# Kernel tuning notes

Hardware: AMD Instinct MI355X
Metric: run time of the kernel (lower is better)

## Reference

```python
import jax, jax.numpy as jnp
import numpy as np

N, E, B, F, H = 50000, 600000, 256, 128, 128
RATIO = 0.8
BN_EPS = 1e-5


def _topk_keep(score, batch, mask):
    # Per-graph top-ceil(RATIO*live) selection, expressed as a fixed-size keep mask.
    s = jnp.where(mask, score, -jnp.inf)
    order = jnp.lexsort((-s, batch))  # primary: batch id, secondary: score desc
    rank = jnp.zeros(N, dtype=jnp.int32).at[order].set(jnp.arange(N, dtype=jnp.int32))
    total = jax.ops.segment_sum(jnp.ones(N, dtype=jnp.int32), batch, B)
    starts = jnp.cumsum(total) - total
    r_in_g = (rank - starts[batch]).astype(jnp.float32)  # rank within own graph
    live = jax.ops.segment_sum(mask.astype(jnp.float32), batch, B)
    k = jnp.ceil(RATIO * live)
    return (r_in_g < k[batch]) & mask


def _forward(x, edge_index, batch, W1s, b1s, W2s, b2s, gammas, betas, pool_ws):
    src, dst = edge_index[0], edge_index[1]
    mask = jnp.ones(N, dtype=bool)      # live-node mask (TopK pooling shrinks graphs)
    e_mask = jnp.ones(E, dtype=bool)    # live-edge mask
    out = jnp.zeros((B, 2 * H), dtype=x.dtype)
    for i in range(4):
        # GINConv (eps=0): MLP(x + sum_{j->i} x_j)
        msg = jnp.where(e_mask[:, None], x[src], 0.0)
        agg = jax.ops.segment_sum(msg, dst, num_segments=N)
        h = x + agg
        h = jax.nn.relu(h @ W1s[i] + b1s[i]) @ W2s[i] + b2s[i]
        # BatchNorm (training mode) over live nodes only
        m = mask[:, None].astype(h.dtype)
        n = jnp.maximum(jnp.sum(m), 1.0)
        mean = jnp.sum(h * m, axis=0) / n
        var = jnp.sum(((h - mean) ** 2) * m, axis=0) / n
        h = (h - mean) * jax.lax.rsqrt(var + BN_EPS) * gammas[i] + betas[i]
        h = jax.nn.relu(h) * m
        # TopKPooling(ratio=0.8): score = x@w/||w||, keep top-k per graph, scale by tanh
        w = pool_ws[i]
        score = (h @ w) / jnp.linalg.norm(w)
        keep = _topk_keep(score, batch, mask)
        x = jnp.where(keep[:, None], h * jnp.tanh(score)[:, None], 0.0)
        mask = keep
        e_mask = e_mask & keep[src] & keep[dst]
        # global max pool + global mean pool over live nodes
        mx = jax.ops.segment_max(jnp.where(mask[:, None], x, -jnp.inf), batch, num_segments=B)
        mx = jnp.where(jnp.isfinite(mx), mx, 0.0)
        cnt = jax.ops.segment_sum(mask.astype(x.dtype), batch, num_segments=B)
        mn = jax.ops.segment_sum(x, batch, num_segments=B) / jnp.maximum(cnt, 1.0)[:, None]
        out = out + jnp.concatenate([mx, mn], axis=1)  # x1 + x2 + x3 + x4
    return out


def setup_inputs() -> dict:
    key = jax.random.key(0)
    k = jax.random.split(key, 8)
    s = 1.0 / np.sqrt(H)
    return {
        "x": jax.random.normal(k[0], (N, F), jnp.float32),
        "edge_index": jax.random.randint(k[1], (2, E), 0, N),
        "batch": jnp.sort(jax.random.randint(k[2], (N,), 0, B)),
        "W1s": jax.random.normal(k[3], (4, F, H), jnp.float32) * s,
        "b1s": jax.random.normal(k[4], (4, H), jnp.float32) * s,
        "W2s": jax.random.normal(k[5], (4, H, H), jnp.float32) * s,
        "b2s": jax.random.normal(k[6], (4, H), jnp.float32) * s,
        "gammas": jnp.ones((4, H), jnp.float32),
        "betas": jnp.zeros((4, H), jnp.float32),
        "pool_ws": jax.random.normal(k[7], (4, H), jnp.float32) * s,
    }


def reference(x, edge_index, batch, W1s, b1s, W2s, b2s, gammas, betas, pool_ws):
    return _forward(x, edge_index, batch, W1s, b1s, W2s, b2s, gammas, betas, pool_ws)
```

## Files before the change

kernel.cpp:

```cpp
#include <hip/hip_runtime.h>
#include <hip/hip_bf16.h>
#include <math.h>


#define HF 128
#define CHUNK_LG 14

typedef __attribute__((ext_vector_type(8))) short short8;
typedef __attribute__((ext_vector_type(4))) float floatx4;

__device__ __forceinline__ unsigned short cvt_bf16(float f) {
    unsigned u = __float_as_uint(f);
    u = u + 0x7fffu + ((u >> 16) & 1u);
    return (unsigned short)(u >> 16);
}
__device__ __forceinline__ float bf16f(unsigned short h) {
    return __uint_as_float(((unsigned)h) << 16);
}


__global__ __launch_bounds__(256)
void k_hist(const int* __restrict__ dst, unsigned int* __restrict__ partial,
            unsigned char* __restrict__ eslot, int* __restrict__ mask,
            float* __restrict__ stats4, float* __restrict__ out,
            int* __restrict__ lc,
            int N, int E, int nd4, int outsz, int X) {
    __shared__ unsigned int lh[12544];
    int bl = blockIdx.x, tid = threadIdx.x;
    for (int i = tid; i < nd4; i += 256) lh[i] = 0;
    __syncthreads();
    int e0 = bl << CHUNK_LG;
    int e1 = min(E, e0 + (1 << CHUNK_LG));
    for (int e = e0 + tid; e < e1; e += 256) {
        int d = dst[e];
        unsigned int old = atomicAdd(&lh[d >> 2], 1u << (8 * (d & 3)));
        eslot[e] = (unsigned char)((old >> (8 * (d & 3))) & 255u);
    }
    __syncthreads();
    for (int i = tid; i < nd4; i += 256) partial[(size_t)bl * nd4 + i] = lh[i];
    int gt = bl * 256 + tid, tot = X * 256;
    for (int i = gt; i < N; i += tot) mask[i] = 1;
    for (int i = gt; i < 4 * 256; i += tot) stats4[i] = 0.f;
    for (int i = gt; i < outsz; i += tot) out[i] = 0.f;
    if (gt < 5) lc[gt] = (gt == 0) ? N : 0;
}

__global__ __launch_bounds__(256)
void k_colsum(const unsigned int* __restrict__ partial, unsigned int* __restrict__ baseoff,
              int* __restrict__ deg, int* __restrict__ blocksum,
              int nd4, int X, int N) {
    __shared__ int red[256];
    int tid = threadIdx.x;
    int d4 = blockIdx.x * 256 + tid;
    unsigned int run = 0;
    if (d4 < nd4) {
        for (int bl = 0; bl < X; ++bl) {
            unsigned int c = partial[(size_t)bl * nd4 + d4];
            baseoff[(size_t)bl * nd4 + d4] = run;
            run += c;
        }
        int d = d4 * 4;
#pragma unroll
        for (int j = 0; j < 4; ++j)
            if (d + j < N) deg[d + j] = (int)((run >> (8 * j)) & 255u);
    }
    int tsum = (int)((run & 255u) + ((run >> 8) & 255u) + ((run >> 16) & 255u) + ((run >> 24) & 255u));
    red[tid] = tsum;
    __syncthreads();
    for (int off = 128; off; off >>= 1) {
        if (tid < off) red[tid] += red[tid + off];
        __syncthreads();
    }
    if (tid == 0) blocksum[blockIdx.x] = red[0];
}

__global__ void k_mid(const int* __restrict__ blocksum, int* __restrict__ blockoff,
                      int nblk, const int* __restrict__ batch,
                      int* __restrict__ gstart, int B, int n) {
    int t = threadIdx.x;
    if (t <= B) {
        int lo = 0, hi = n;
        while (lo < hi) { int mid = (lo + hi) >> 1; if (batch[mid] < t) lo = mid + 1; else hi = mid; }
        gstart[t] = lo;
    }
    if (t < 64) {
        int b0 = (t < nblk) ? blocksum[t] : 0;
        int v = b0;
#pragma unroll
        for (int off = 1; off < 64; off <<= 1) {
            int u = __shfl_up(v, off, 64);
            if (t >= off) v += u;
        }
        if (t < nblk) blockoff[t] = v - b0;
    }
}

__global__ __launch_bounds__(256)
void k_indptr(const int* __restrict__ deg, const int* __restrict__ blockoff,
              int* __restrict__ indptr, int nd4, int N) {
    __shared__ int ss[256];
    int tid = threadIdx.x;
    int d4 = blockIdx.x * 256 + tid;
    int dv[4] = {0, 0, 0, 0};
    int tsum = 0;
    if (d4 < nd4) {
        int d = d4 * 4;
#pragma unroll
        for (int j = 0; j < 4; ++j)
            if (d + j < N) { dv[j] = deg[d + j]; tsum += dv[j]; }
    }
    ss[tid] = tsum;
    __syncthreads();
    for (int off = 1; off < 256; off <<= 1) {
        int v = (tid >= off) ? ss[tid - off] : 0;
        __syncthreads();
        ss[tid] += v;
        __syncthreads();
    }
    if (d4 < nd4) {
        int b = blockoff[blockIdx.x] + ss[tid] - tsum;
        int d = d4 * 4;
#pragma unroll
        for (int j = 0; j < 4; ++j)
            if (d + j < N) { indptr[d + j] = b; b += dv[j]; }
        if (d4 == (N - 1) >> 2) indptr[N] = b;
    }
}

__global__ __launch_bounds__(256)
void k_place(const int* __restrict__ src, const int* __restrict__ dst,
             const unsigned char* __restrict__ eslot, const unsigned int* __restrict__ baseoff,
             const int* __restrict__ indptr, int* __restrict__ csr, int E, int nd4) {
    int e = blockIdx.x * 256 + threadIdx.x;
    if (e >= E) return;
    int d = dst[e];
    int bl = e >> CHUNK_LG;
    unsigned int bo = (baseoff[(size_t)bl * nd4 + (d >> 2)] >> (8 * (d & 3))) & 255u;
    csr[indptr[d] + (int)bo + (int)eslot[e]] = src[e];
}

__global__ void k_wsplit(const float* __restrict__ W1s, const float* __restrict__ W2s,
                         short8* __restrict__ wf) {
    int t = blockIdx.x * 256 + threadIdx.x;
    if (t >= 4 * 2 * 4 * 8 * 64) return;
    int lane = t & 63; int r = t >> 6;
    int ct = r & 7; r >>= 3; int kc = r & 3; r >>= 2; int g = r & 1; int l = r >> 1;
    const float* W = (g ? W2s : W1s) + l * 16384;
    int m = lane & 15, q = lane >> 4;
    int col = ct * 16 + m;
    short8 v1, v2, v3;
#pragma unroll
    for (int j = 0; j < 8; ++j) {
        float f = W[(size_t)(kc * 32 + q * 8 + j) * HF + col];
        unsigned short p1 = cvt_bf16(f); float r1 = f - bf16f(p1);
        unsigned short p2 = cvt_bf16(r1); float r2 = r1 - bf16f(p2);
        unsigned short p3 = cvt_bf16(r2);
        v1[j] = (short)p1; v2[j] = (short)p2; v3[j] = (short)p3;
    }
    size_t base = ((size_t)(l * 2 + g) * 6144) + ((size_t)(kc * 8 + ct) * 64) + lane;
    wf[base] = v1; wf[base + 2048] = v2; wf[base + 4096] = v3;
}


__global__ __launch_bounds__(256)
void k_agg(const float* __restrict__ x, const int* __restrict__ indptr,
           const int* __restrict__ csr, float* __restrict__ xa,
           const int* __restrict__ ll, const int* __restrict__ cnt, int N) {
    int widx = (blockIdx.x * 256 + threadIdx.x) >> 6;
    int count = ll ? *cnt : N;
    if (widx >= count) return;
    int wid = ll ? ll[widx] : widx;
    int lane = threadIdx.x & 63;
    int half = lane >> 5;
    int c = (lane & 31) * 4;
    int beg = indptr[wid], end = indptr[wid + 1];
    float4 a0 = make_float4(0.f, 0.f, 0.f, 0.f), a1 = a0, a2 = a0, a3 = a0;
    int e = beg + half;
    for (; e + 6 < end; e += 8) {
        int s0 = csr[e], s1 = csr[e + 2], s2 = csr[e + 4], s3 = csr[e + 6];
        float4 v0 = *(const float4*)&x[(size_t)s0 * HF + c];
        float4 v1 = *(const float4*)&x[(size_t)s1 * HF + c];
        float4 v2 = *(const float4*)&x[(size_t)s2 * HF + c];
        float4 v3 = *(const float4*)&x[(size_t)s3 * HF + c];
        a0.x += v0.x; a0.y += v0.y; a0.z += v0.z; a0.w += v0.w;
        a1.x += v1.x; a1.y += v1.y; a1.z += v1.z; a1.w += v1.w;
        a2.x += v2.x; a2.y += v2.y; a2.z += v2.z; a2.w += v2.w;
        a3.x += v3.x; a3.y += v3.y; a3.z += v3.z; a3.w += v3.w;
    }
    for (; e < end; e += 2) {
        int s0 = csr[e];
        float4 v0 = *(const float4*)&x[(size_t)s0 * HF + c];
        a0.x += v0.x; a0.y += v0.y; a0.z += v0.z; a0.w += v0.w;
    }
    float4 acc = make_float4(a0.x + a1.x + a2.x + a3.x, a0.y + a1.y + a2.y + a3.y,
                             a0.z + a1.z + a2.z + a3.z, a0.w + a1.w + a2.w + a3.w);
    acc.x += __shfl_down(acc.x, 32);
    acc.y += __shfl_down(acc.y, 32);
    acc.z += __shfl_down(acc.z, 32);
    acc.w += __shfl_down(acc.w, 32);
    if (half == 0) {
        float4 xv = *(const float4*)&x[(size_t)wid * HF + c];
        acc.x += xv.x; acc.y += xv.y; acc.z += xv.z; acc.w += xv.w;
        *(float4*)&xa[(size_t)wid * HF + c] = acc;
    }
}

__global__ __launch_bounds__(256, 4)
void k_mlp(const float* __restrict__ xa,
           const short8* __restrict__ wf1, const short8* __restrict__ wf2,
           const float* __restrict__ b1, const float* __restrict__ b2,
           const int* __restrict__ ll, const int* __restrict__ cnt,
           float* __restrict__ h, float* __restrict__ stats, int N) {
    __shared__ float sIn[4 * 16 * 132];
    int tid = threadIdx.x;
    int count = ll ? *cnt : N;
    if (blockIdx.x * 64 >= count) return;
    int w = tid >> 6, lane = tid & 63;
    int m = lane & 15, q = lane >> 4;
    int base = blockIdx.x * 64 + w * 16;
    float* sR = &sIn[w * 16 * 132];

#pragma unroll
    for (int it = 0; it < 8; ++it) {
        int slot = it * 64 + lane;
        int r = slot >> 5, kq = slot & 31;
        int idx = base + r;
        float4 v = make_float4(0.f, 0.f, 0.f, 0.f);
        if (idx < count) {
            int row = ll ? ll[idx] : idx;
            v = *(const float4*)&xa[(size_t)row * HF + kq * 4];
        }
        *(float4*)&sR[r * 132 + kq * 4] = v;
    }
    __syncthreads();

    floatx4 acc[8];
#pragma unroll
    for (int ct = 0; ct < 8; ++ct) acc[ct] = (floatx4){0.f, 0.f, 0.f, 0.f};

#pragma unroll
    for (int kc = 0; kc < 4; ++kc) {
        const float* ap = &sR[m * 132 + kc * 32 + q * 8];
        float4 x0 = *(const float4*)ap;
        float4 x1 = *(const float4*)(ap + 4);
        float av[8] = {x0.x, x0.y, x0.z, x0.w, x1.x, x1.y, x1.z, x1.w};
        short8 a1v, a2v, a3v;
#pragma unroll
        for (int j = 0; j < 8; ++j) {
            float f = av[j];
            unsigned short p1 = cvt_bf16(f); float r1 = f - bf16f(p1);
            unsigned short p2 = cvt_bf16(r1); float r2 = r1 - bf16f(p2);
            unsigned short p3 = cvt_bf16(r2);
            a1v[j] = (short)p1; a2v[j] = (short)p2; a3v[j] = (short)p3;
        }
#pragma unroll
        for (int ct = 0; ct < 8; ++ct) {
            const short8* bp = wf1 + (size_t)(kc * 8 + ct) * 64 + lane;
            short8 bf1 = bp[0], bf2 = bp[2048], bf3 = bp[4096];
            acc[ct] = __builtin_amdgcn_mfma_f32_16x16x32_bf16(a1v, bf1, acc[ct], 0, 0, 0);
            acc[ct] = __builtin_amdgcn_mfma_f32_16x16x32_bf16(a2v, bf1, acc[ct], 0, 0, 0);
            acc[ct] = __builtin_amdgcn_mfma_f32_16x16x32_bf16(a1v, bf2, acc[ct], 0, 0, 0);
            acc[ct] = __builtin_amdgcn_mfma_f32_16x16x32_bf16(a3v, bf1, acc[ct], 0, 0, 0);
            acc[ct] = __builtin_amdgcn_mfma_f32_16x16x32_bf16(a2v, bf2, acc[ct], 0, 0, 0);
            acc[ct] = __builtin_amdgcn_mfma_f32_16x16x32_bf16(a1v, bf3, acc[ct], 0, 0, 0);
        }
    }

    float bb1[8];
#pragma unroll
    for (int ct = 0; ct < 8; ++ct) bb1[ct] = b1[ct * 16 + m];
#pragma unroll
    for (int ct = 0; ct < 8; ++ct) {
#pragma unroll
        for (int reg = 0; reg < 4; ++reg) {
            float v = fmaxf(acc[ct][reg] + bb1[ct], 0.f);
            sR[(q * 4 + reg) * 132 + ct * 16 + m] = v;
        }
        acc[ct] = (floatx4){0.f, 0.f, 0.f, 0.f};
    }
    __syncthreads();

#pragma unroll
    for (int kc = 0; kc < 4; ++kc) {
        const float* ap = &sR[m * 132 + kc * 32 + q * 8];
        float4 x0 = *(const float4*)ap;
        float4 x1 = *(const float4*)(ap + 4);
        float av[8] = {x0.x, x0.y, x0.z, x0.w, x1.x, x1.y, x1.z, x1.w};
        short8 a1v, a2v, a3v;
#pragma unroll
        for (int j = 0; j < 8; ++j) {
            float f = av[j];
            unsigned short p1 = cvt_bf16(f); float r1 = f - bf16f(p1);
            unsigned short p2 = cvt_bf16(r1); float r2 = r1 - bf16f(p2);
            unsigned short p3 = cvt_bf16(r2);
            a1v[j] = (short)p1; a2v[j] = (short)p2; a3v[j] = (short)p3;
        }
#pragma unroll
        for (int ct = 0; ct < 8; ++ct) {
            const short8* bp = wf2 + (size_t)(kc * 8 + ct) * 64 + lane;
            short8 bf1 = bp[0], bf2 = bp[2048], bf3 = bp[4096];
            acc[ct] = __builtin_amdgcn_mfma_f32_16x16x32_bf16(a1v, bf1, acc[ct], 0, 0, 0);
            acc[ct] = __builtin_amdgcn_mfma_f32_16x16x32_bf16(a2v, bf1, acc[ct], 0, 0, 0);
            acc[ct] = __builtin_amdgcn_mfma_f32_16x16x32_bf16(a1v, bf2, acc[ct], 0, 0, 0);
            acc[ct] = __builtin_amdgcn_mfma_f32_16x16x32_bf16(a3v, bf1, acc[ct], 0, 0, 0);
            acc[ct] = __builtin_amdgcn_mfma_f32_16x16x32_bf16(a2v, bf2, acc[ct], 0, 0, 0);
            acc[ct] = __builtin_amdgcn_mfma_f32_16x16x32_bf16(a1v, bf3, acc[ct], 0, 0, 0);
        }
    }

    float bb2[8];
#pragma unroll
    for (int ct = 0; ct < 8; ++ct) bb2[ct] = b2[ct * 16 + m];
    int rowv[4];
#pragma unroll
    for (int reg = 0; reg < 4; ++reg) {
        int idx = base + q * 4 + reg;
        rowv[reg] = (idx < count) ? (ll ? ll[idx] : idx) : -1;
    }
    float sv[8], qv[8];
#pragma unroll
    for (int ct = 0; ct < 8; ++ct) {
        float s = 0.f, qq = 0.f;
#pragma unroll
        for (int reg = 0; reg < 4; ++reg) {
            float v = acc[ct][reg] + bb2[ct];
            if (rowv[reg] >= 0) {
                h[(size_t)rowv[reg] * HF + ct * 16 + m] = v;
                s += v; qq += v * v;
            }
        }
        s += __shfl_xor(s, 16, 64);  s += __shfl_xor(s, 32, 64);
        qq += __shfl_xor(qq, 16, 64); qq += __shfl_xor(qq, 32, 64);
        sv[ct] = s; qv[ct] = qq;
    }
    __syncthreads();
    float* sStat = sIn;
    if (lane < 16) {
#pragma unroll
        for (int ct = 0; ct < 8; ++ct) {
            sStat[w * 256 + ct * 16 + lane] = sv[ct];
            sStat[1024 + w * 256 + ct * 16 + lane] = qv[ct];
        }
    }
    __syncthreads();
    if (tid < 128) {
        float s = sStat[tid] + sStat[256 + tid] + sStat[512 + tid] + sStat[768 + tid];
        float qq = sStat[1024 + tid] + sStat[1280 + tid] + sStat[1536 + tid] + sStat[1792 + tid];
        atomicAdd(&stats[tid], s);
        atomicAdd(&stats[128 + tid], qq);
    }
}

__global__ __launch_bounds__(512)
void k_topkpool(const float* __restrict__ h, const float* __restrict__ stats,
                const float* __restrict__ gamma, const float* __restrict__ beta,
                const float* __restrict__ w, int* __restrict__ mask,
                const int* __restrict__ gstart, float* __restrict__ x,
                float* __restrict__ out, const int* __restrict__ cnt_in,
                int* __restrict__ ll_out, int* __restrict__ lcnt_out, int N) {
    __shared__ unsigned long long skey[512];
    __shared__ float sscore[512];
    __shared__ float sscale[128], sshift[128], swv[128], sred[128];
    __shared__ float smx[3 * 128], ssum[3 * 128];
    __shared__ int s_live, s_base;
    int b = blockIdx.x, tid = threadIdx.x;
    int gs = gstart[b], ge = gstart[b + 1];
    int size = ge - gs;
    if (size > 512) size = 512;
    int M = (size <= 256) ? 256 : 512;
    if (tid == 0) s_live = 0;
    if (tid < 128) { float wc = w[tid]; swv[tid] = wc; sred[tid] = wc * wc; }
    __syncthreads();
    for (int off = 64; off; off >>= 1) {
        if (tid < off) sred[tid] += sred[tid + off];
        __syncthreads();
    }
    float normv = sqrtf(sred[0]);
    if (tid < 128) {
        float n = fmaxf((float)(*cnt_in), 1.0f);
        float mean = stats[tid] / n;
        float var = fmaxf(stats[128 + tid] / n - mean * mean, 0.f);
        float sc = gamma[tid] * rsqrtf(var + 1e-5f);
        sscale[tid] = sc;
        sshift[tid] = beta[tid] - mean * sc;
    }
    __syncthreads();

    int wv = tid >> 6, lane = tid & 63;
    int lc = 0;
    for (int j = wv; j < M; j += 8) {
        unsigned long long key = (0xFFFFFFFFull << 32) | (unsigned)j;
        bool live = (j < size) && (mask[gs + j] != 0);
        if (live) {
            int c = lane * 2;
            float2 v = *(const float2*)&h[(size_t)(gs + j) * HF + c];
            float a0 = fmaxf(fmaf(v.x, sscale[c], sshift[c]), 0.f);
            float a1 = fmaxf(fmaf(v.y, sscale[c + 1], sshift[c + 1]), 0.f);
            float s = a0 * swv[c] + a1 * swv[c + 1];
#pragma unroll
            for (int off = 32; off; off >>= 1) s += __shfl_down(s, off, 64);
            if (lane == 0) {
                float scv = s / normv;
                sscore[j] = scv;
                unsigned u = __float_as_uint(scv);
                u = (u & 0x80000000u) ? ~u : (u | 0x80000000u);
                key = (((unsigned long long)(~u)) << 32) | (unsigned)j;
            }
        }
        if (lane == 0) { skey[j] = key; if (live) lc++; }
    }
    if (lane == 0 && lc) atomicAdd(&s_live, lc);
    __syncthreads();

    for (int k = 2; k <= M; k <<= 1) {
        for (int jj = k >> 1; jj > 0; jj >>= 1) {
            for (int t = tid; t < M; t += 512) {
                int ixj = t ^ jj;
                if (ixj > t) {
                    bool up = ((t & k) == 0);
                    unsigned long long A = skey[t], Bv = skey[ixj];
                    if ((A > Bv) == up) { skey[t] = Bv; skey[ixj] = A; }
                }
            }
            __syncthreads();
        }
    }
    int live = s_live;
    int kk = (live > 0) ? (int)ceilf(0.8f * (float)live) : 0;

    if (tid == 0 && ll_out) s_base = atomicAdd(lcnt_out, kk);
    for (int j = tid; j < size; j += 512) sscore[j] = tanhf(sscore[j]);
    __syncthreads();
    if (ll_out) {
        for (int p = tid; p < kk; p += 512)
            ll_out[s_base + p] = gs + (int)(skey[p] & 0xFFFFFFFFu);
    }

    int f = tid & 127, hf = tid >> 7;
    float mx = -INFINITY, sum = 0.f;
    for (int p = hf; p < live; p += 4) {
        int local = (int)(skey[p] & 0xFFFFFFFFu);
        int node = gs + local;
        float v = 0.f;
        bool keep = (p < kk);
        if (keep) {
            float hv = h[(size_t)node * HF + f];
            hv = fmaxf(fmaf(hv, sscale[f], sshift[f]), 0.f);
            v = hv * sscore[local];
            mx = fmaxf(mx, v);
            sum += v;
        }
        x[(size_t)node * HF + f] = v;
        if (f == 0) mask[node] = keep ? 1 : 0;
    }
    if (hf) { smx[(hf - 1) * 128 + f] = mx; ssum[(hf - 1) * 128 + f] = sum; }
    __syncthreads();
    if (hf == 0) {
#pragma unroll
        for (int k2 = 0; k2 < 3; ++k2) {
            mx = fmaxf(mx, smx[k2 * 128 + f]);
            sum += ssum[k2 * 128 + f];
        }
        float mxo = (kk > 0) ? mx : 0.f;
        float mn = sum / (float)(kk > 0 ? kk : 1);
        out[b * 256 + f] += mxo;
        out[b * 256 + 128 + f] += mn;
    }
}


extern "C" void kernel_launch(void* const* d_in, const int* in_sizes, int n_in,
                              void* d_out, int out_size, void* d_ws, size_t ws_size,
                              hipStream_t stream) {
    const float* x_in    = (const float*)d_in[0];
    const int*   ei      = (const int*)d_in[1];
    const int*   batch   = (const int*)d_in[2];
    const float* W1s     = (const float*)d_in[3];
    const float* b1s     = (const float*)d_in[4];
    const float* W2s     = (const float*)d_in[5];
    const float* b2s     = (const float*)d_in[6];
    const float* gammas  = (const float*)d_in[7];
    const float* betas   = (const float*)d_in[8];
    const float* pool_ws = (const float*)d_in[9];

    int N = in_sizes[0] / HF;
    int E = in_sizes[1] / 2;
    int B = out_size / (2 * HF);
    const int* src = ei;
    const int* dst = ei + E;
    int nd4 = (N + 3) >> 2;
    int X = (E + (1 << CHUNK_LG) - 1) >> CHUNK_LG;
    int nblk = (nd4 + 255) >> 8;

    char* ws = (char*)d_ws;
    size_t off = 0;
    auto alloc = [&](size_t bytes) -> void* {
        void* p = ws + off;
        off = (off + bytes + 255) & ~(size_t)255;
        return p;
    };
    float* xa      = (float*)alloc((size_t)N * HF * 4);
    float* h       = (float*)alloc((size_t)N * HF * 4);
    float* xbuf    = (float*)alloc((size_t)N * HF * 4);
    int*   mask    = (int*)alloc((size_t)N * 4);
    int*   deg     = (int*)alloc((size_t)(N + 1) * 4);
    int*   indptr  = (int*)alloc((size_t)(N + 1) * 4);
    int*   csr     = (int*)alloc((size_t)E * 4);
    int*   gstart  = (int*)alloc((size_t)(B + 1) * 4);
    float* stats4  = (float*)alloc(4 * 256 * 4);
    int*   lc      = (int*)alloc(8 * 4);
    int*   llA     = (int*)alloc((size_t)N * 4);
    int*   llB     = (int*)alloc((size_t)N * 4);
    int*   blocksum = (int*)alloc(64 * 4);
    int*   blockoff = (int*)alloc(64 * 4);
    short8* wfrag  = (short8*)alloc((size_t)8 * 6144 * 16);
    unsigned int* partial = (unsigned int*)alloc((size_t)X * nd4 * 4);
    unsigned int* baseoff = (unsigned int*)alloc((size_t)X * nd4 * 4);
    unsigned char* eslot  = (unsigned char*)alloc((size_t)E);
    float* out    = (float*)d_out;

    int tb = 256;
    k_hist<<<X, tb, 0, stream>>>(dst, partial, eslot, mask, stats4, out, lc,
                                 N, E, nd4, out_size, X);
    k_wsplit<<<64, tb, 0, stream>>>(W1s, W2s, wfrag);
    k_colsum<<<nblk, tb, 0, stream>>>(partial, baseoff, deg, blocksum, nd4, X, N);
    k_mid<<<1, 512, 0, stream>>>(blocksum, blockoff, nblk, batch, gstart, B, N);
    k_indptr<<<nblk, tb, 0, stream>>>(deg, blockoff, indptr, nd4, N);
    k_place<<<(E + tb - 1) / tb, tb, 0, stream>>>(src, dst, eslot, baseoff, indptr, csr, E, nd4);

    int bound[4];
    bound[0] = N;
    for (int i = 1; i < 4; ++i) bound[i] = (4 * bound[i - 1] + 4) / 5 + B;

    const int* ll_in[4] = {nullptr, llA, llB, llA};
    int*       ll_ot[4] = {llA, llB, llA, llB};

    for (int i = 0; i < 4; ++i) {
        const float* xc = (i == 0) ? x_in : xbuf;
        float* stats = stats4 + i * 256;
        k_agg<<<(bound[i] + 3) / 4, tb, 0, stream>>>(xc, indptr, csr, xa,
                                                     ll_in[i], lc + i, N);
        k_mlp<<<(bound[i] + 63) / 64, tb, 0, stream>>>(xa,
                                                wfrag + (size_t)(i * 2) * 6144,
                                                wfrag + (size_t)(i * 2 + 1) * 6144,
                                                b1s + i * 128, b2s + i * 128,
                                                ll_in[i], lc + i, h, stats, N);
        k_topkpool<<<B, 512, 0, stream>>>(h, stats, gammas + i * 128, betas + i * 128,
                                          pool_ws + i * 128, mask, gstart, xbuf, out,
                                          lc + i, ll_ot[i], lc + i + 1, N);
    }
}
```

Before: 622.9 us.

## Process two row tiles per wave in MLP kernel with register-prefetched operands

```diff
diff --git a/kernel.cpp b/kernel.cpp
--- a/kernel.cpp
+++ b/kernel.cpp
@@ -16,6 +16,17 @@
 }
 __device__ __forceinline__ float bf16f(unsigned short h) {
     return __uint_as_float(((unsigned)h) << 16);
+}
+
+__device__ __forceinline__ void split3(float f, short& p1, short& p2, short& p3) {
+    unsigned u = __float_as_uint(f);
+    unsigned r = u + 0x7fffu + ((u >> 16) & 1u);
+    p1 = (short)(r >> 16);
+    float r1 = f - __uint_as_float(r & 0xffff0000u);
+    unsigned u1 = __float_as_uint(r1);
+    p2 = (short)(u1 >> 16);
+    float r2 = r1 - __uint_as_float(u1 & 0xffff0000u);
+    p3 = (short)(__float_as_uint(r2) >> 16);
 }
 
 
@@ -205,136 +216,169 @@
     }
 }
 
-__global__ __launch_bounds__(256, 4)
+__global__ __launch_bounds__(256, 2)
 void k_mlp(const float* __restrict__ xa,
            const short8* __restrict__ wf1, const short8* __restrict__ wf2,
            const float* __restrict__ b1, const float* __restrict__ b2,
            const int* __restrict__ ll, const int* __restrict__ cnt,
            float* __restrict__ h, float* __restrict__ stats, int N) {
-    __shared__ float sIn[4 * 16 * 132];
+    __shared__ float sH[4 * 2 * 16 * 132];
     int tid = threadIdx.x;
     int count = ll ? *cnt : N;
-    if (blockIdx.x * 64 >= count) return;
+    if (blockIdx.x * 128 >= count) return;
     int w = tid >> 6, lane = tid & 63;
     int m = lane & 15, q = lane >> 4;
-    int base = blockIdx.x * 64 + w * 16;
-    float* sR = &sIn[w * 16 * 132];
-
-#pragma unroll
-    for (int it = 0; it < 8; ++it) {
-        int slot = it * 64 + lane;
-        int r = slot >> 5, kq = slot & 31;
-        int idx = base + r;
-        float4 v = make_float4(0.f, 0.f, 0.f, 0.f);
-        if (idx < count) {
-            int row = ll ? ll[idx] : idx;
-            v = *(const float4*)&xa[(size_t)row * HF + kq * 4];
-        }
-        *(float4*)&sR[r * 132 + kq * 4] = v;
-    }
-    __syncthreads();
-
-    floatx4 acc[8];
-#pragma unroll
-    for (int ct = 0; ct < 8; ++ct) acc[ct] = (floatx4){0.f, 0.f, 0.f, 0.f};
-
-#pragma unroll
+    int base = blockIdx.x * 128 + w * 32;
+
+    const float* aptr[2];
+#pragma unroll
+    for (int t = 0; t < 2; ++t) {
+        int idx = base + t * 16 + m;
+        int idc = (idx < count) ? idx : (count - 1);
+        int row = ll ? ll[idc] : idc;
+        aptr[t] = &xa[(size_t)row * HF + q * 8];
+    }
+
+    floatx4 acc[2][8];
+#pragma unroll
+    for (int t = 0; t < 2; ++t)
+#pragma unroll
+        for (int ct = 0; ct < 8; ++ct) acc[t][ct] = (floatx4){0.f, 0.f, 0.f, 0.f};
+
+    float4 af0[2], af1[2];
+#pragma unroll
+    for (int t = 0; t < 2; ++t) {
+        af0[t] = *(const float4*)(aptr[t]);
+        af1[t] = *(const float4*)(aptr[t] + 4);
+    }
+#pragma unroll 1
     for (int kc = 0; kc < 4; ++kc) {
-        const float* ap = &sR[m * 132 + kc * 32 + q * 8];
-        float4 x0 = *(const float4*)ap;
-        float4 x1 = *(const float4*)(ap + 4);
-        float av[8] = {x0.x, x0.y, x0.z, x0.w, x1.x, x1.y, x1.z, x1.w};
-        short8 a1v, a2v, a3v;
-#pragma unroll
-        for (int j = 0; j < 8; ++j) {
-            float f = av[j];
-            unsigned short p1 = cvt_bf16(f); float r1 = f - bf16f(p1);
-            unsigned short p2 = cvt_bf16(r1); float r2 = r1 - bf16f(p2);
-            unsigned short p3 = cvt_bf16(r2);
-            a1v[j] = (short)p1; a2v[j] = (short)p2; a3v[j] = (short)p3;
-        }
+        short8 as[2][3];
+#pragma unroll
+        for (int t = 0; t < 2; ++t) {
+            float av[8] = {af0[t].x, af0[t].y, af0[t].z, af0[t].w,
+                           af1[t].x, af1[t].y, af1[t].z, af1[t].w};
+#pragma unroll
+            for (int j = 0; j < 8; ++j) {
+                short p1, p2, p3;
+                split3(av[j], p1, p2, p3);
+                as[t][0][j] = p1; as[t][1][j] = p2; as[t][2][j] = p3;
+            }
+        }
+        if (kc < 3) {
+#pragma unroll
+            for (int t = 0; t < 2; ++t) {
+                af0[t] = *(const float4*)(aptr[t] + (kc + 1) * 32);
+                af1[t] = *(const float4*)(aptr[t] + (kc + 1) * 32 + 4);
+            }
+        }
+        const short8* bp = wf1 + (size_t)(kc * 8) * 64 + lane;
+        short8 c1 = bp[0], c2 = bp[2048], c3 = bp[4096];
 #pragma unroll
         for (int ct = 0; ct < 8; ++ct) {
-            const short8* bp = wf1 + (size_t)(kc * 8 + ct) * 64 + lane;
-            short8 bf1 = bp[0], bf2 = bp[2048], bf3 = bp[4096];
-            acc[ct] = __builtin_amdgcn_mfma_f32_16x16x32_bf16(a1v, bf1, acc[ct], 0, 0, 0);
-            acc[ct] = __builtin_amdgcn_mfma_f32_16x16x32_bf16(a2v, bf1, acc[ct], 0, 0, 0);
-            acc[ct] = __builtin_amdgcn_mfma_f32_16x16x32_bf16(a1v, bf2, acc[ct], 0, 0, 0);
-            acc[ct] = __builtin_amdgcn_mfma_f32_16x16x32_bf16(a3v, bf1, acc[ct], 0, 0, 0);
-            acc[ct] = __builtin_amdgcn_mfma_f32_16x16x32_bf16(a2v, bf2, acc[ct], 0, 0, 0);
-            acc[ct] = __builtin_amdgcn_mfma_f32_16x16x32_bf16(a1v, bf3, acc[ct], 0, 0, 0);
-        }
-    }
-
+            short8 n1, n2, n3;
+            if (ct < 7) {
+                const short8* np = bp + (size_t)(ct + 1) * 64;
+                n1 = np[0]; n2 = np[2048]; n3 = np[4096];
+            }
+#pragma unroll
+            for (int t = 0; t < 2; ++t) {
+                acc[t][ct] = __builtin_amdgcn_mfma_f32_16x16x32_bf16(as[t][0], c1, acc[t][ct], 0, 0, 0);
+                acc[t][ct] = __builtin_amdgcn_mfma_f32_16x16x32_bf16(as[t][1], c1, acc[t][ct], 0, 0, 0);
+                acc[t][ct] = __builtin_amdgcn_mfma_f32_16x16x32_bf16(as[t][0], c2, acc[t][ct], 0, 0, 0);
+                acc[t][ct] = __builtin_amdgcn_mfma_f32_16x16x32_bf16(as[t][2], c1, acc[t][ct], 0, 0, 0);
+                acc[t][ct] = __builtin_amdgcn_mfma_f32_16x16x32_bf16(as[t][1], c2, acc[t][ct], 0, 0, 0);
+                acc[t][ct] = __builtin_amdgcn_mfma_f32_16x16x32_bf16(as[t][0], c3, acc[t][ct], 0, 0, 0);
+            }
+            if (ct < 7) { c1 = n1; c2 = n2; c3 = n3; }
+        }
+    }
+
+    float* sl[2] = {&sH[(w * 2) * 16 * 132], &sH[(w * 2 + 1) * 16 * 132]};
     float bb1[8];
 #pragma unroll
     for (int ct = 0; ct < 8; ++ct) bb1[ct] = b1[ct * 16 + m];
 #pragma unroll
-    for (int ct = 0; ct < 8; ++ct) {
+    for (int t = 0; t < 2; ++t)
+#pragma unroll
+        for (int ct = 0; ct < 8; ++ct) {
+#pragma unroll
+            for (int reg = 0; reg < 4; ++reg) {
+                float v = fmaxf(acc[t][ct][reg] + bb1[ct], 0.f);
+                sl[t][(q * 4 + reg) * 132 + ct * 16 + m] = v;
+            }
+            acc[t][ct] = (floatx4){0.f, 0.f, 0.f, 0.f};
+        }
+
+#pragma unroll 1
+    for (int kc = 0; kc < 4; ++kc) {
+        short8 as[2][3];
+#pragma unroll
+        for (int t = 0; t < 2; ++t) {
+            const float* ap = &sl[t][m * 132 + kc * 32 + q * 8];
+            float4 x0 = *(const float4*)ap;
+            float4 x1 = *(const float4*)(ap + 4);
+            float av[8] = {x0.x, x0.y, x0.z, x0.w, x1.x, x1.y, x1.z, x1.w};
+#pragma unroll
+            for (int j = 0; j < 8; ++j) {
+                short p1, p2, p3;
+                split3(av[j], p1, p2, p3);
+                as[t][0][j] = p1; as[t][1][j] = p2; as[t][2][j] = p3;
+            }
+        }
+        const short8* bp = wf2 + (size_t)(kc * 8) * 64 + lane;
+        short8 c1 = bp[0], c2 = bp[2048], c3 = bp[4096];
+#pragma unroll
+        for (int ct = 0; ct < 8; ++ct) {
+            short8 n1, n2, n3;
+            if (ct < 7) {
+                const short8* np = bp + (size_t)(ct + 1) * 64;
+                n1 = np[0]; n2 = np[2048]; n3 = np[4096];
+            }
+#pragma unroll
+            for (int t = 0; t < 2; ++t) {
+                acc[t][ct] = __builtin_amdgcn_mfma_f32_16x16x32_bf16(as[t][0], c1, acc[t][ct], 0, 0, 0);
+                acc[t][ct] = __builtin_amdgcn_mfma_f32_16x16x32_bf16(as[t][1], c1, acc[t][ct], 0, 0, 0);
+                acc[t][ct] = __builtin_amdgcn_mfma_f32_16x16x32_bf16(as[t][0], c2, acc[t][ct], 0, 0, 0);
+                acc[t][ct] = __builtin_amdgcn_mfma_f32_16x16x32_bf16(as[t][2], c1, acc[t][ct], 0, 0, 0);
+                acc[t][ct] = __builtin_amdgcn_mfma_f32_16x16x32_bf16(as[t][1], c2, acc[t][ct], 0, 0, 0);
+                acc[t][ct] = __builtin_amdgcn_mfma_f32_16x16x32_bf16(as[t][0], c3, acc[t][ct], 0, 0, 0);
+            }
+            if (ct < 7) { c1 = n1; c2 = n2; c3 = n3; }
+        }
+    }
+
+    float bb2[8];
+#pragma unroll
+    for (int ct = 0; ct < 8; ++ct) bb2[ct] = b2[ct * 16 + m];
+    int rowv[2][4];
+#pragma unroll
+    for (int t = 0; t < 2; ++t)
 #pragma unroll
         for (int reg = 0; reg < 4; ++reg) {
-            float v = fmaxf(acc[ct][reg] + bb1[ct], 0.f);
-            sR[(q * 4 + reg) * 132 + ct * 16 + m] = v;
-        }
-        acc[ct] = (floatx4){0.f, 0.f, 0.f, 0.f};
-    }
-    __syncthreads();
-
-#pragma unroll
-    for (int kc = 0; kc < 4; ++kc) {
-        const float* ap = &sR[m * 132 + kc * 32 + q * 8];
-        float4 x0 = *(const float4*)ap;
-        float4 x1 = *(const float4*)(ap + 4);
-        float av[8] = {x0.x, x0.y, x0.z, x0.w, x1.x, x1.y, x1.z, x1.w};
-        short8 a1v, a2v, a3v;
-#pragma unroll
-        for (int j = 0; j < 8; ++j) {
-            float f = av[j];
-            unsigned short p1 = cvt_bf16(f); float r1 = f - bf16f(p1);
-            unsigned short p2 = cvt_bf16(r1); float r2 = r1 - bf16f(p2);
-            unsigned short p3 = cvt_bf16(r2);
-            a1v[j] = (short)p1; a2v[j] = (short)p2; a3v[j] = (short)p3;
-        }
-#pragma unroll
-        for (int ct = 0; ct < 8; ++ct) {
-            const short8* bp = wf2 + (size_t)(kc * 8 + ct) * 64 + lane;
-            short8 bf1 = bp[0], bf2 = bp[2048], bf3 = bp[4096];
-            acc[ct] = __builtin_amdgcn_mfma_f32_16x16x32_bf16(a1v, bf1, acc[ct], 0, 0, 0);
-            acc[ct] = __builtin_amdgcn_mfma_f32_16x16x32_bf16(a2v, bf1, acc[ct], 0, 0, 0);
-            acc[ct] = __builtin_amdgcn_mfma_f32_16x16x32_bf16(a1v, bf2, acc[ct], 0, 0, 0);
-            acc[ct] = __builtin_amdgcn_mfma_f32_16x16x32_bf16(a3v, bf1, acc[ct], 0, 0, 0);
-            acc[ct] = __builtin_amdgcn_mfma_f32_16x16x32_bf16(a2v, bf2, acc[ct], 0, 0, 0);
-            acc[ct] = __builtin_amdgcn_mfma_f32_16x16x32_bf16(a1v, bf3, acc[ct], 0, 0, 0);
-        }
-    }
-
-    float bb2[8];
-#pragma unroll
-    for (int ct = 0; ct < 8; ++ct) bb2[ct] = b2[ct * 16 + m];
-    int rowv[4];
-#pragma unroll
-    for (int reg = 0; reg < 4; ++reg) {
-        int idx = base + q * 4 + reg;
-        rowv[reg] = (idx < count) ? (ll ? ll[idx] : idx) : -1;
-    }
+            int idx = base + t * 16 + q * 4 + reg;
+            rowv[t][reg] = (idx < count) ? (ll ? ll[idx] : idx) : -1;
+        }
     float sv[8], qv[8];
 #pragma unroll
     for (int ct = 0; ct < 8; ++ct) {
         float s = 0.f, qq = 0.f;
 #pragma unroll
-        for (int reg = 0; reg < 4; ++reg) {
-            float v = acc[ct][reg] + bb2[ct];
-            if (rowv[reg] >= 0) {
-                h[(size_t)rowv[reg] * HF + ct * 16 + m] = v;
-                s += v; qq += v * v;
-            }
-        }
+        for (int t = 0; t < 2; ++t)
+#pragma unroll
+            for (int reg = 0; reg < 4; ++reg) {
+                float v = acc[t][ct][reg] + bb2[ct];
+                if (rowv[t][reg] >= 0) {
+                    h[(size_t)rowv[t][reg] * HF + ct * 16 + m] = v;
+                    s += v; qq += v * v;
+                }
+            }
         s += __shfl_xor(s, 16, 64);  s += __shfl_xor(s, 32, 64);
         qq += __shfl_xor(qq, 16, 64); qq += __shfl_xor(qq, 32, 64);
         sv[ct] = s; qv[ct] = qq;
     }
     __syncthreads();
-    float* sStat = sIn;
+    float* sStat = sH;
     if (lane < 16) {
 #pragma unroll
         for (int ct = 0; ct < 8; ++ct) {
@@ -540,7 +584,7 @@
         float* stats = stats4 + i * 256;
         k_agg<<<(bound[i] + 3) / 4, tb, 0, stream>>>(xc, indptr, csr, xa,
                                                      ll_in[i], lc + i, N);
-        k_mlp<<<(bound[i] + 63) / 64, tb, 0, stream>>>(xa,
+        k_mlp<<<(bound[i] + 127) / 128, tb, 0, stream>>>(xa,
                                                 wfrag + (size_t)(i * 2) * 6144,
                                                 wfrag + (size_t)(i * 2 + 1) * 6144,
                                                 b1s + i * 128, b2s + i * 128,
```

Result: faster. 582.2 us (-6.5%).
